# Kernel tuning notes

Hardware: AMD Instinct MI355X
Metric: run time of the kernel (lower is better)

## Reference

```python
import jax, jax.numpy as jnp
import numpy as np

STRIDE, PAD, DIL = 1, 1, 1

def _bilinear_sample(inp_flat, py, px, H, W, dtype):
    # inp_flat: [B, C, H*W]; py/px: [B, K, Ho, Wo] float sampling positions
    y0 = jnp.floor(py); x0 = jnp.floor(px)
    ly = py - y0; lx = px - x0
    y0i = y0.astype(jnp.int32); x0i = x0.astype(jnp.int32)

    def gather(yi, xi):
        valid = (yi >= 0) & (yi < H) & (xi >= 0) & (xi < W)
        idx = jnp.clip(yi, 0, H - 1) * W + jnp.clip(xi, 0, W - 1)  # [B,K,Ho,Wo]
        vals = jax.vmap(lambda xf, ix: xf[:, ix])(inp_flat, idx)    # [B,C,K,Ho,Wo]
        return vals * valid[:, None].astype(dtype)

    out = ((1 - ly) * (1 - lx))[:, None] * gather(y0i, x0i)
    out = out + ((1 - ly) * lx)[:, None] * gather(y0i, x0i + 1)
    out = out + (ly * (1 - lx))[:, None] * gather(y0i + 1, x0i)
    out = out + (ly * lx)[:, None] * gather(y0i + 1, x0i + 1)
    return out  # [B, C, K, Ho, Wo]

def setup_inputs() -> dict:
    key = jax.random.key(0)
    k1, k2, k3, k4 = jax.random.split(key, 4)
    B, Cin, Cout, H, W, kh, kw = 8, 128, 128, 64, 64, 3, 3
    n = Cin * kh * kw
    stdv = 1.0 / np.sqrt(n)
    inp = jax.random.normal(k1, (B, Cin, H, W), dtype=jnp.float32)
    offset = jax.random.normal(k2, (B, 2 * kh * kw, H, W), dtype=jnp.float32)
    mask = jax.random.uniform(k3, (B, kh * kw, H, W), dtype=jnp.float32)
    weight = jax.random.uniform(k4, (Cout, Cin, kh, kw), dtype=jnp.float32,
                                minval=-stdv, maxval=stdv)
    bias = jnp.zeros((Cout,), dtype=jnp.float32)
    return {"input": inp, "offset": offset, "mask": mask, "weight": weight, "bias": bias}

def reference(input, offset, mask, weight, bias):
    B, C, H, W = input.shape
    Cout, Cin, kh, kw = weight.shape
    K = kh * kw
    Ho = (H + 2 * PAD - DIL * (kh - 1) - 1) // STRIDE + 1
    Wo = (W + 2 * PAD - DIL * (kw - 1) - 1) // STRIDE + 1
    dtype = input.dtype

    # Offset channel layout (DCNv2): channel 2k = dy, 2k+1 = dx for kernel tap k
    off_y = offset[:, 0::2]  # [B, K, Ho, Wo]
    off_x = offset[:, 1::2]

    ky, kx = jnp.meshgrid(jnp.arange(kh), jnp.arange(kw), indexing="ij")
    ky = (ky.reshape(-1) * DIL).astype(dtype)  # [K]
    kx = (kx.reshape(-1) * DIL).astype(dtype)
    base_y = (jnp.arange(Ho) * STRIDE - PAD).astype(dtype)  # [Ho]
    base_x = (jnp.arange(Wo) * STRIDE - PAD).astype(dtype)

    py = off_y + base_y[None, None, :, None] + ky[None, :, None, None]  # [B,K,Ho,Wo]
    px = off_x + base_x[None, None, None, :] + kx[None, :, None, None]

    inp_flat = input.reshape(B, C, H * W)
    sampled = _bilinear_sample(inp_flat, py, px, H, W, dtype)  # [B,C,K,Ho,Wo]
    cols = sampled * mask[:, None]                              # modulation

    w2 = weight.reshape(Cout, Cin * K)
    cols2 = cols.reshape(B, Cin * K, Ho * Wo)
    out = jnp.einsum("om,bmp->bop", w2, cols2).reshape(B, Cout, Ho, Wo)
    return out + bias[None, :, None, None]
```

## Files before the change

### kernel.cpp

```cpp
#include <hip/hip_runtime.h>


constexpr int CIN = 128, COUT = 128, H = 64, W = 64, KK = 9;
constexpr int HW = H * W;

typedef __attribute__((ext_vector_type(8))) short short8;
typedef __attribute__((ext_vector_type(4))) float float4v;

static __device__ __forceinline__ unsigned short f32_to_bf16_rne(float f) {
  unsigned u = __float_as_uint(f);
  return (unsigned short)((u + 0x7FFFu + ((u >> 16) & 1u)) >> 16);
}
static __device__ __forceinline__ float blo(unsigned u) {
  return __uint_as_float(u << 16);
}
static __device__ __forceinline__ float bhi(unsigned u) {
  return __uint_as_float(u & 0xFFFF0000u);
}

__global__ __launch_bounds__(256) void tprep_kernel(
    const float* __restrict__ in, unsigned short* __restrict__ inT) {
  __shared__ unsigned short lt[64 * 130];
  const int b = blockIdx.x >> 6, y = blockIdx.x & 63;
  for (int i = threadIdx.x; i < 128 * 64; i += 256) {
    const int ci = i >> 6, x = i & 63;
    lt[x * 130 + ci] = f32_to_bf16_rne(in[((b * 128 + ci) * 64 + y) * 64 + x]);
  }
  __syncthreads();
  unsigned* outp = (unsigned*)inT + (size_t)(b * 64 + y) * 64 * 64;
  for (int i = threadIdx.x; i < 64 * 64; i += 256) {
    const int x = i >> 6, c2 = (i & 63) * 2;
    outp[x * 64 + (i & 63)] =
        (unsigned)lt[x * 130 + c2] | ((unsigned)lt[x * 130 + c2 + 1] << 16);
  }
}

__global__ __launch_bounds__(256) void wprep_kernel(
    const float* __restrict__ w, unsigned short* __restrict__ wt) {
  const int t = blockIdx.x * 256 + threadIdx.x;
  if (t >= 9 * 4 * 8 * 64) return;
  const int lane = t & 63, c16 = (t >> 6) & 7, kt = t >> 9;
  const int ks = kt & 3, k = kt >> 2;
  const int co = c16 * 16 + (lane & 15);
  const int ci0 = ks * 32 + (lane >> 4) * 8;
  unsigned pk[4];
#pragma unroll
  for (int jj = 0; jj < 4; ++jj) {
    const unsigned short h0 =
        f32_to_bf16_rne(w[(co * CIN + ci0 + 2 * jj) * KK + k]);
    const unsigned short h1 =
        f32_to_bf16_rne(w[(co * CIN + ci0 + 2 * jj + 1) * KK + k]);
    pk[jj] = (unsigned)h0 | ((unsigned)h1 << 16);
  }
  *(uint4*)(wt + (size_t)t * 8) = make_uint4(pk[0], pk[1], pk[2], pk[3]);
}

__global__ __launch_bounds__(256, 4) void dcn_mfma_kernel(
    const unsigned short* __restrict__ inT, const float* __restrict__ offset,
    const float* __restrict__ mask, const unsigned short* __restrict__ wt,
    const float* __restrict__ bias, float* __restrict__ out) {
  __shared__ int2 pos_i[KK * 32];
  __shared__ float4 pos_w[KK * 32];
  __shared__ unsigned short s_t[2][32 * 128];

  const int b = blockIdx.x & 7;
  const int ho = (blockIdx.x >> 3) & 63;
  const int ph = blockIdx.x >> 9;
  const int tid = threadIdx.x;

  for (int idx = tid; idx < KK * 32; idx += 256) {
    const int k = idx >> 5, p = idx & 31;
    const int pg = ph * 32 + p;
    const int ky = k / 3, kx = k - 3 * ky;
    const float py = (float)(ho - 1 + ky) +
                     offset[((b * 18 + 2 * k) * 64 + ho) * 64 + pg];
    const float px = (float)(pg - 1 + kx) +
                     offset[((b * 18 + 2 * k + 1) * 64 + ho) * 64 + pg];
    const float m = mask[((b * 9 + k) * 64 + ho) * 64 + pg];
    const float y0f = floorf(py), x0f = floorf(px);
    const int y0 = (int)y0f, x0 = (int)x0f;
    const float ly = py - y0f, lx = px - x0f;
    const float hy = 1.f - ly, hx = 1.f - lx;
    const bool vy0 = (y0 >= 0) && (y0 < H);
    const bool vy1 = (y0 + 1 >= 0) && (y0 + 1 < H);
    const bool vx0 = (x0 >= 0) && (x0 < W);
    const bool vx1 = (x0 + 1 >= 0) && (x0 + 1 < W);
    const float w00 = (vy0 && vx0) ? hy * hx * m : 0.f;
    const float w01 = (vy0 && vx1) ? hy * lx * m : 0.f;
    const float w10 = (vy1 && vx0) ? ly * hx * m : 0.f;
    const float w11 = (vy1 && vx1) ? ly * lx * m : 0.f;
    const int cy0 = min(max(y0, 0), H - 1), cy1 = min(max(y0 + 1, 0), H - 1);
    const int bx = min(max(x0, 0), W - 2);
    const int s0 = min(max(x0 - bx, 0), 1);
    const int s1 = min(max(x0 + 1 - bx, 0), 1);
    const float cA0 = (s0 == 0 ? w00 : 0.f) + (s1 == 0 ? w01 : 0.f);
    const float cB0 = (s0 == 1 ? w00 : 0.f) + (s1 == 1 ? w01 : 0.f);
    const float cA1 = (s0 == 0 ? w10 : 0.f) + (s1 == 0 ? w11 : 0.f);
    const float cB1 = (s0 == 1 ? w10 : 0.f) + (s1 == 1 ? w11 : 0.f);
    pos_i[idx] = make_int2((cy0 * 64 + bx) * 128, (cy1 * 64 + bx) * 128);
    pos_w[idx] = make_float4(cA0, cB0, cA1, cB1);
  }
  __syncthreads();

  const int wave = tid >> 6;
  const int lane = tid & 63;
  const int quad = lane >> 4, l15 = lane & 15;
  const int p_loc = tid >> 3;
  const int cg8 = tid & 7;

  float4v acc[2][2];
#pragma unroll
  for (int s = 0; s < 2; ++s)
#pragma unroll
    for (int n = 0; n < 2; ++n) acc[s][n] = (float4v)(0.f);

  const unsigned short* inb = inT + (size_t)b * HW * 128;

  int2 P = pos_i[p_loc];
  float4 Wc = pos_w[p_loc];
  uint4 ga0, ga1, gb0, gb1, gc0, gc1, gd0, gd1;
  {
    const unsigned short* a0 = inb + P.x + cg8 * 16;
    const unsigned short* a1 = inb + P.y + cg8 * 16;
    ga0 = *(const uint4*)a0;
    ga1 = *(const uint4*)(a0 + 8);
    gb0 = *(const uint4*)(a0 + 128);
    gb1 = *(const uint4*)(a0 + 136);
    gc0 = *(const uint4*)a1;
    gc1 = *(const uint4*)(a1 + 8);
    gd0 = *(const uint4*)(a1 + 128);
    gd1 = *(const uint4*)(a1 + 136);
  }

  for (int k = 0; k < KK; ++k) {
    const int buf = k & 1;
    {
      const uint4 A4[2] = {ga0, ga1}, B4[2] = {gb0, gb1};
      const uint4 C4[2] = {gc0, gc1}, D4[2] = {gd0, gd1};
#pragma unroll
      for (int h = 0; h < 2; ++h) {
        const unsigned u00[4] = {A4[h].x, A4[h].y, A4[h].z, A4[h].w};
        const unsigned u01[4] = {B4[h].x, B4[h].y, B4[h].z, B4[h].w};
        const unsigned u10[4] = {C4[h].x, C4[h].y, C4[h].z, C4[h].w};
        const unsigned u11[4] = {D4[h].x, D4[h].y, D4[h].z, D4[h].w};
        unsigned pk[4];
#pragma unroll
        for (int j = 0; j < 4; ++j) {
          const float se = Wc.x * blo(u00[j]) + Wc.y * blo(u01[j]) +
                           Wc.z * blo(u10[j]) + Wc.w * blo(u11[j]);
          const float so = Wc.x * bhi(u00[j]) + Wc.y * bhi(u01[j]) +
                           Wc.z * bhi(u10[j]) + Wc.w * bhi(u11[j]);
          pk[j] = (unsigned)f32_to_bf16_rne(se) |
                  ((unsigned)f32_to_bf16_rne(so) << 16);
        }
        const int gi = cg8 * 2 + h;
        const int pgr = gi ^ (p_loc & 7);
        *(uint4*)&s_t[buf][p_loc * 128 + pgr * 8] =
            make_uint4(pk[0], pk[1], pk[2], pk[3]);
      }
    }
    __syncthreads();

    short8 A[4][2];
    {
      const unsigned short* wk =
          wt + ((size_t)(k * 4) * 8 + wave * 2) * 512 + (size_t)lane * 8;
#pragma unroll
      for (int ks = 0; ks < 4; ++ks) {
        A[ks][0] = *(const short8*)(wk + (size_t)ks * 8 * 512);
        A[ks][1] = *(const short8*)(wk + (size_t)ks * 8 * 512 + 512);
      }
    }

    if (k < KK - 1) {
      P = pos_i[(k + 1) * 32 + p_loc];
      Wc = pos_w[(k + 1) * 32 + p_loc];
      const unsigned short* a0 = inb + P.x + cg8 * 16;
      const unsigned short* a1 = inb + P.y + cg8 * 16;
      ga0 = *(const uint4*)a0;
      ga1 = *(const uint4*)(a0 + 8);
      gb0 = *(const uint4*)(a0 + 128);
      gb1 = *(const uint4*)(a0 + 136);
      gc0 = *(const uint4*)a1;
      gc1 = *(const uint4*)(a1 + 8);
      gd0 = *(const uint4*)(a1 + 128);
      gd1 = *(const uint4*)(a1 + 136);
    }

#pragma unroll
    for (int ks = 0; ks < 4; ++ks) {
      const int gi = ks * 4 + quad;
      const int o0 = l15 * 128 + (gi ^ (l15 & 7)) * 8;
      const int o1 = (16 + l15) * 128 + (gi ^ (l15 & 7)) * 8;
      const short8 b0 = *(const short8*)&s_t[buf][o0];
      const short8 b1 = *(const short8*)&s_t[buf][o1];
      acc[0][0] =
          __builtin_amdgcn_mfma_f32_16x16x32_bf16(A[ks][0], b0, acc[0][0], 0, 0, 0);
      acc[0][1] =
          __builtin_amdgcn_mfma_f32_16x16x32_bf16(A[ks][0], b1, acc[0][1], 0, 0, 0);
      acc[1][0] =
          __builtin_amdgcn_mfma_f32_16x16x32_bf16(A[ks][1], b0, acc[1][0], 0, 0, 0);
      acc[1][1] =
          __builtin_amdgcn_mfma_f32_16x16x32_bf16(A[ks][1], b1, acc[1][1], 0, 0, 0);
    }
  }

#pragma unroll
  for (int sub = 0; sub < 2; ++sub) {
#pragma unroll
    for (int r = 0; r < 4; ++r) {
      const int co = wave * 32 + sub * 16 + quad * 4 + r;
      const float bb = bias[co];
      float* op = out + ((size_t)(b * COUT + co) * H + ho) * W + ph * 32;
      op[l15] = acc[sub][0][r] + bb;
      op[16 + l15] = acc[sub][1][r] + bb;
    }
  }
}

__global__ __launch_bounds__(256) void dcn_fp32_kernel(
    const float* __restrict__ input, const float* __restrict__ offset,
    const float* __restrict__ mask, const float* __restrict__ weight,
    const float* __restrict__ bias, float* __restrict__ out) {
  __shared__ short4 pos_o[KK * 64];
  __shared__ float4 pos_w[KK * 64];
  __shared__ float s_tile[64 * 64];
  __shared__ float w_tile[64 * 128];
  const int b = blockIdx.x >> 6;
  const int ho = blockIdx.x & 63;
  const int tid = threadIdx.x;
  for (int idx = tid; idx < KK * 64; idx += 256) {
    const int k = idx >> 6, pp = idx & 63;
    const int ky = k / 3, kx = k - 3 * ky;
    const float py = (float)(ho - 1 + ky) +
                     offset[((b * 18 + 2 * k) * 64 + ho) * 64 + pp];
    const float px = (float)(pp - 1 + kx) +
                     offset[((b * 18 + 2 * k + 1) * 64 + ho) * 64 + pp];
    const float m = mask[((b * 9 + k) * 64 + ho) * 64 + pp];
    const float y0f = floorf(py), x0f = floorf(px);
    const int y0 = (int)y0f, x0 = (int)x0f;
    const float ly = py - y0f, lx = px - x0f;
    const float hy = 1.f - ly, hx = 1.f - lx;
    const bool vy0 = (y0 >= 0) && (y0 < H), vy1 = (y0 + 1 >= 0) && (y0 + 1 < H);
    const bool vx0 = (x0 >= 0) && (x0 < W), vx1 = (x0 + 1 >= 0) && (x0 + 1 < W);
    const int cy0 = min(max(y0, 0), H - 1), cy1 = min(max(y0 + 1, 0), H - 1);
    const int cx0 = min(max(x0, 0), W - 1), cx1 = min(max(x0 + 1, 0), W - 1);
    pos_o[idx] = make_short4((short)(cy0 * W + cx0), (short)(cy0 * W + cx1),
                             (short)(cy1 * W + cx0), (short)(cy1 * W + cx1));
    pos_w[idx] = make_float4((vy0 && vx0) ? hy * hx * m : 0.f,
                             (vy0 && vx1) ? hy * lx * m : 0.f,
                             (vy1 && vx0) ? ly * hx * m : 0.f,
                             (vy1 && vx1) ? ly * lx * m : 0.f);
  }
  const int cog = tid >> 4, pg = tid & 15;
  float acc[8][4];
#pragma unroll
  for (int j = 0; j < 8; ++j)
#pragma unroll
    for (int q = 0; q < 4; ++q) acc[j][q] = 0.f;
  const float* inp_b = input + (size_t)b * CIN * HW;
  for (int k = 0; k < KK; ++k) {
    for (int cc = 0; cc < 2; ++cc) {
      __syncthreads();
      for (int i = tid; i < 64 * 64; i += 256) {
        const int cil = i >> 6, pp = i & 63;
        const float* plane = inp_b + (size_t)(cc * 64 + cil) * HW;
        const short4 o = pos_o[k * 64 + pp];
        const float4 w = pos_w[k * 64 + pp];
        s_tile[i] = w.x * plane[(int)o.x] + w.y * plane[(int)o.y] +
                    w.z * plane[(int)o.z] + w.w * plane[(int)o.w];
      }
      for (int i = tid; i < 64 * 128; i += 256) {
        const int cil = i & 63, co = i >> 6;
        w_tile[cil * 128 + co] = weight[(co * CIN + cc * 64 + cil) * KK + k];
      }
      __syncthreads();
#pragma unroll 8
      for (int cil = 0; cil < 64; ++cil) {
        const float4 sv = *(const float4*)&s_tile[cil * 64 + (pg << 2)];
        const float4 wa = *(const float4*)&w_tile[cil * 128 + (cog << 3)];
        const float4 wb = *(const float4*)&w_tile[cil * 128 + (cog << 3) + 4];
        const float s4[4] = {sv.x, sv.y, sv.z, sv.w};
        const float w8[8] = {wa.x, wa.y, wa.z, wa.w, wb.x, wb.y, wb.z, wb.w};
#pragma unroll
        for (int j = 0; j < 8; ++j)
#pragma unroll
          for (int q = 0; q < 4; ++q) acc[j][q] = fmaf(w8[j], s4[q], acc[j][q]);
      }
    }
  }
  float* outp = out + (size_t)b * COUT * HW + ho * W;
#pragma unroll
  for (int j = 0; j < 8; ++j) {
    const int co = (cog << 3) + j;
    const float bb = bias[co];
    *(float4*)&outp[co * HW + (pg << 2)] =
        make_float4(acc[j][0] + bb, acc[j][1] + bb, acc[j][2] + bb,
                    acc[j][3] + bb);
  }
}

extern "C" void kernel_launch(void* const* d_in, const int* in_sizes, int n_in,
                              void* d_out, int out_size, void* d_ws,
                              size_t ws_size, hipStream_t stream) {
  const float* input = (const float*)d_in[0];
  const float* offset = (const float*)d_in[1];
  const float* mask = (const float*)d_in[2];
  const float* weight = (const float*)d_in[3];
  const float* bias = (const float*)d_in[4];
  float* out = (float*)d_out;

  const size_t wt_bytes = (size_t)9 * 4 * 8 * 64 * 8 * 2;
  const size_t inT_bytes = (size_t)8 * HW * 128 * 2;
  if (ws_size >= wt_bytes + inT_bytes) {
    unsigned short* wt = (unsigned short*)d_ws;
    unsigned short* inT = (unsigned short*)((char*)d_ws + wt_bytes);
    hipLaunchKernelGGL(wprep_kernel, dim3(72), dim3(256), 0, stream, weight, wt);
    hipLaunchKernelGGL(tprep_kernel, dim3(512), dim3(256), 0, stream, input, inT);
    hipLaunchKernelGGL(dcn_mfma_kernel, dim3(1024), dim3(256), 0, stream, inT,
                       offset, mask, wt, bias, out);
  } else {
    hipLaunchKernelGGL(dcn_fp32_kernel, dim3(512), dim3(256), 0, stream, input,
                       offset, mask, weight, bias, out);
  }
}
```

Baseline: 107.4 us.

## Warp-specialize DCN kernel into producer sampling waves and consumer MFMA waves

Splits the block's four waves into two roles. Waves 0-1 gather and bilinearly blend the sampled input into double-buffered LDS, running one tap ahead. Waves 2-3 run the bf16 MFMA GEMM over that buffer, with each consumer wave now covering 64 output channels. The aim is to overlap gather latency with matrix math across waves rather than inside each wave. In exchange, each producer thread handles twice the gather work, each consumer thread holds twice the accumulators (more register pressure), and half the waves no longer issue MFMAs.

New measurement: 116.3 us. 1.08x slower.

```diff
diff --git a/kernel.cpp b/kernel.cpp
--- a/kernel.cpp
+++ b/kernel.cpp
@@ -103,117 +103,147 @@
   __syncthreads();
 
   const int wave = tid >> 6;
-  const int lane = tid & 63;
-  const int quad = lane >> 4, l15 = lane & 15;
-  const int p_loc = tid >> 3;
-  const int cg8 = tid & 7;
-
-  float4v acc[2][2];
-#pragma unroll
-  for (int s = 0; s < 2; ++s)
-#pragma unroll
-    for (int n = 0; n < 2; ++n) acc[s][n] = (float4v)(0.f);
-
   const unsigned short* inb = inT + (size_t)b * HW * 128;
 
-  int2 P = pos_i[p_loc];
-  float4 Wc = pos_w[p_loc];
-  uint4 ga0, ga1, gb0, gb1, gc0, gc1, gd0, gd1;
-  {
-    const unsigned short* a0 = inb + P.x + cg8 * 16;
-    const unsigned short* a1 = inb + P.y + cg8 * 16;
-    ga0 = *(const uint4*)a0;
-    ga1 = *(const uint4*)(a0 + 8);
-    gb0 = *(const uint4*)(a0 + 128);
-    gb1 = *(const uint4*)(a0 + 136);
-    gc0 = *(const uint4*)a1;
-    gc1 = *(const uint4*)(a1 + 8);
-    gd0 = *(const uint4*)(a1 + 128);
-    gd1 = *(const uint4*)(a1 + 136);
-  }
-
-  for (int k = 0; k < KK; ++k) {
-    const int buf = k & 1;
+  if (wave < 2) {
+    const int p = tid >> 2;
+    const int cgr = tid & 3;
+    const int coff = cgr * 32;
+    uint4 g00[4], g01[4], g10[4], g11[4];
+    float4 Wc;
+
     {
-      const uint4 A4[2] = {ga0, ga1}, B4[2] = {gb0, gb1};
-      const uint4 C4[2] = {gc0, gc1}, D4[2] = {gd0, gd1};
-#pragma unroll
-      for (int h = 0; h < 2; ++h) {
-        const unsigned u00[4] = {A4[h].x, A4[h].y, A4[h].z, A4[h].w};
-        const unsigned u01[4] = {B4[h].x, B4[h].y, B4[h].z, B4[h].w};
-        const unsigned u10[4] = {C4[h].x, C4[h].y, C4[h].z, C4[h].w};
-        const unsigned u11[4] = {D4[h].x, D4[h].y, D4[h].z, D4[h].w};
-        unsigned pk[4];
-#pragma unroll
-        for (int j = 0; j < 4; ++j) {
-          const float se = Wc.x * blo(u00[j]) + Wc.y * blo(u01[j]) +
-                           Wc.z * blo(u10[j]) + Wc.w * blo(u11[j]);
-          const float so = Wc.x * bhi(u00[j]) + Wc.y * bhi(u01[j]) +
-                           Wc.z * bhi(u10[j]) + Wc.w * bhi(u11[j]);
-          pk[j] = (unsigned)f32_to_bf16_rne(se) |
-                  ((unsigned)f32_to_bf16_rne(so) << 16);
+      const int2 P = pos_i[p];
+      Wc = pos_w[p];
+      const unsigned short* a0 = inb + P.x + coff;
+      const unsigned short* a1 = inb + P.y + coff;
+#pragma unroll
+      for (int q = 0; q < 4; ++q) {
+        g00[q] = *(const uint4*)(a0 + q * 8);
+        g01[q] = *(const uint4*)(a0 + 128 + q * 8);
+        g10[q] = *(const uint4*)(a1 + q * 8);
+        g11[q] = *(const uint4*)(a1 + 128 + q * 8);
+      }
+    }
+#pragma unroll
+    for (int q = 0; q < 4; ++q) {
+      const unsigned u00[4] = {g00[q].x, g00[q].y, g00[q].z, g00[q].w};
+      const unsigned u01[4] = {g01[q].x, g01[q].y, g01[q].z, g01[q].w};
+      const unsigned u10[4] = {g10[q].x, g10[q].y, g10[q].z, g10[q].w};
+      const unsigned u11[4] = {g11[q].x, g11[q].y, g11[q].z, g11[q].w};
+      unsigned pk[4];
+#pragma unroll
+      for (int c = 0; c < 4; ++c) {
+        const float se = Wc.x * blo(u00[c]) + Wc.y * blo(u01[c]) +
+                         Wc.z * blo(u10[c]) + Wc.w * blo(u11[c]);
+        const float so = Wc.x * bhi(u00[c]) + Wc.y * bhi(u01[c]) +
+                         Wc.z * bhi(u10[c]) + Wc.w * bhi(u11[c]);
+        pk[c] = (unsigned)f32_to_bf16_rne(se) |
+                ((unsigned)f32_to_bf16_rne(so) << 16);
+      }
+      const int sg = (cgr * 4 + q) ^ (p & 7);
+      *(uint4*)&s_t[0][p * 128 + sg * 8] = make_uint4(pk[0], pk[1], pk[2], pk[3]);
+    }
+    {
+      const int2 P = pos_i[32 + p];
+      Wc = pos_w[32 + p];
+      const unsigned short* a0 = inb + P.x + coff;
+      const unsigned short* a1 = inb + P.y + coff;
+#pragma unroll
+      for (int q = 0; q < 4; ++q) {
+        g00[q] = *(const uint4*)(a0 + q * 8);
+        g01[q] = *(const uint4*)(a0 + 128 + q * 8);
+        g10[q] = *(const uint4*)(a1 + q * 8);
+        g11[q] = *(const uint4*)(a1 + 128 + q * 8);
+      }
+    }
+    __syncthreads();
+
+    for (int t = 0; t < KK; ++t) {
+      if (t < KK - 1) {
+#pragma unroll
+        for (int q = 0; q < 4; ++q) {
+          const unsigned u00[4] = {g00[q].x, g00[q].y, g00[q].z, g00[q].w};
+          const unsigned u01[4] = {g01[q].x, g01[q].y, g01[q].z, g01[q].w};
+          const unsigned u10[4] = {g10[q].x, g10[q].y, g10[q].z, g10[q].w};
+          const unsigned u11[4] = {g11[q].x, g11[q].y, g11[q].z, g11[q].w};
+          unsigned pk[4];
+#pragma unroll
+          for (int c = 0; c < 4; ++c) {
+            const float se = Wc.x * blo(u00[c]) + Wc.y * blo(u01[c]) +
+                             Wc.z * blo(u10[c]) + Wc.w * blo(u11[c]);
+            const float so = Wc.x * bhi(u00[c]) + Wc.y * bhi(u01[c]) +
+                             Wc.z * bhi(u10[c]) + Wc.w * bhi(u11[c]);
+            pk[c] = (unsigned)f32_to_bf16_rne(se) |
+                    ((unsigned)f32_to_bf16_rne(so) << 16);
+          }
+          const int sg = (cgr * 4 + q) ^ (p & 7);
+          *(uint4*)&s_t[(t + 1) & 1][p * 128 + sg * 8] =
+              make_uint4(pk[0], pk[1], pk[2], pk[3]);
         }
-        const int gi = cg8 * 2 + h;
-        const int pgr = gi ^ (p_loc & 7);
-        *(uint4*)&s_t[buf][p_loc * 128 + pgr * 8] =
-            make_uint4(pk[0], pk[1], pk[2], pk[3]);
-      }
-    }
+        if (t < KK - 2) {
+          const int2 P = pos_i[(t + 2) * 32 + p];
+          Wc = pos_w[(t + 2) * 32 + p];
+          const unsigned short* a0 = inb + P.x + coff;
+          const unsigned short* a1 = inb + P.y + coff;
+#pragma unroll
+          for (int q = 0; q < 4; ++q) {
+            g00[q] = *(const uint4*)(a0 + q * 8);
+            g01[q] = *(const uint4*)(a0 + 128 + q * 8);
+            g10[q] = *(const uint4*)(a1 + q * 8);
+            g11[q] = *(const uint4*)(a1 + 128 + q * 8);
+          }
+        }
+      }
+      __syncthreads();
+    }
+  } else {
+    const int cw = wave - 2;
+    const int lane = tid & 63;
+    const int quad = lane >> 4, l15 = lane & 15;
+
+    float4v acc[4][2];
+#pragma unroll
+    for (int s = 0; s < 4; ++s)
+#pragma unroll
+      for (int n = 0; n < 2; ++n) acc[s][n] = (float4v)(0.f);
+
     __syncthreads();
 
-    short8 A[4][2];
-    {
-      const unsigned short* wk =
-          wt + ((size_t)(k * 4) * 8 + wave * 2) * 512 + (size_t)lane * 8;
+    for (int t = 0; t < KK; ++t) {
+      const int buf = t & 1;
+      const unsigned short* wkbase =
+          wt + ((size_t)t * 32 + cw * 4) * 512 + (size_t)lane * 8;
 #pragma unroll
       for (int ks = 0; ks < 4; ++ks) {
-        A[ks][0] = *(const short8*)(wk + (size_t)ks * 8 * 512);
-        A[ks][1] = *(const short8*)(wk + (size_t)ks * 8 * 512 + 512);
-      }
-    }
-
-    if (k < KK - 1) {
-      P = pos_i[(k + 1) * 32 + p_loc];
-      Wc = pos_w[(k + 1) * 32 + p_loc];
-      const unsigned short* a0 = inb + P.x + cg8 * 16;
-      const unsigned short* a1 = inb + P.y + cg8 * 16;
-      ga0 = *(const uint4*)a0;
-      ga1 = *(const uint4*)(a0 + 8);
-      gb0 = *(const uint4*)(a0 + 128);
-      gb1 = *(const uint4*)(a0 + 136);
-      gc0 = *(const uint4*)a1;
-      gc1 = *(const uint4*)(a1 + 8);
-      gd0 = *(const uint4*)(a1 + 128);
-      gd1 = *(const uint4*)(a1 + 136);
-    }
-
-#pragma unroll
-    for (int ks = 0; ks < 4; ++ks) {
-      const int gi = ks * 4 + quad;
-      const int o0 = l15 * 128 + (gi ^ (l15 & 7)) * 8;
-      const int o1 = (16 + l15) * 128 + (gi ^ (l15 & 7)) * 8;
-      const short8 b0 = *(const short8*)&s_t[buf][o0];
-      const short8 b1 = *(const short8*)&s_t[buf][o1];
-      acc[0][0] =
-          __builtin_amdgcn_mfma_f32_16x16x32_bf16(A[ks][0], b0, acc[0][0], 0, 0, 0);
-      acc[0][1] =
-          __builtin_amdgcn_mfma_f32_16x16x32_bf16(A[ks][0], b1, acc[0][1], 0, 0, 0);
-      acc[1][0] =
-          __builtin_amdgcn_mfma_f32_16x16x32_bf16(A[ks][1], b0, acc[1][0], 0, 0, 0);
-      acc[1][1] =
-          __builtin_amdgcn_mfma_f32_16x16x32_bf16(A[ks][1], b1, acc[1][1], 0, 0, 0);
-    }
-  }
-
-#pragma unroll
-  for (int sub = 0; sub < 2; ++sub) {
-#pragma unroll
-    for (int r = 0; r < 4; ++r) {
-      const int co = wave * 32 + sub * 16 + quad * 4 + r;
-      const float bb = bias[co];
-      float* op = out + ((size_t)(b * COUT + co) * H + ho) * W + ph * 32;
-      op[l15] = acc[sub][0][r] + bb;
-      op[16 + l15] = acc[sub][1][r] + bb;
+        short8 A[4];
+#pragma unroll
+        for (int sub = 0; sub < 4; ++sub)
+          A[sub] = *(const short8*)(wkbase + (size_t)(ks * 8 + sub) * 512);
+        const int swz = ((ks * 4 + quad) ^ (l15 & 7)) * 8;
+        const short8 b0 = *(const short8*)&s_t[buf][l15 * 128 + swz];
+        const short8 b1 = *(const short8*)&s_t[buf][(16 + l15) * 128 + swz];
+#pragma unroll
+        for (int sub = 0; sub < 4; ++sub) {
+          acc[sub][0] = __builtin_amdgcn_mfma_f32_16x16x32_bf16(A[sub], b0,
+                                                               acc[sub][0], 0, 0, 0);
+          acc[sub][1] = __builtin_amdgcn_mfma_f32_16x16x32_bf16(A[sub], b1,
+                                                               acc[sub][1], 0, 0, 0);
+        }
+      }
+      __syncthreads();
+    }
+
+#pragma unroll
+    for (int sub = 0; sub < 4; ++sub) {
+#pragma unroll
+      for (int r = 0; r < 4; ++r) {
+        const int co = cw * 64 + sub * 16 + quad * 4 + r;
+        const float bb = bias[co];
+        float* op = out + ((size_t)(b * COUT + co) * H + ho) * W + ph * 32;
+        op[l15] = acc[sub][0][r] + bb;
+        op[16 + l15] = acc[sub][1][r] + bb;
+      }
     }
   }
 }
```

## Widen DCN MFMA block to full output row with 8 waves

Applied to the files above, without the earlier changes.

Each block now handles a full 64-pixel output row using 512 threads (8 waves) instead of half a row with 256 threads. Each wave computes 16 output channels across all 64 pixels, so it loads half as many weight fragments per tap while covering twice the pixels. The sampling and position tables are shared across the whole row, which halves redundant per-block setup and the block count. The trade-off is more shared memory per block, a smaller grid and fewer independent accumulators per wave, which may lower occupancy or latency hiding.

Measured after the change: 104.9 us. 2.4% less time.

```diff
diff --git a/kernel.cpp b/kernel.cpp
--- a/kernel.cpp
+++ b/kernel.cpp
@@ -55,28 +55,26 @@
   *(uint4*)(wt + (size_t)t * 8) = make_uint4(pk[0], pk[1], pk[2], pk[3]);
 }
 
-__global__ __launch_bounds__(256, 4) void dcn_mfma_kernel(
+__global__ __launch_bounds__(512, 4) void dcn_mfma_kernel(
     const unsigned short* __restrict__ inT, const float* __restrict__ offset,
     const float* __restrict__ mask, const unsigned short* __restrict__ wt,
     const float* __restrict__ bias, float* __restrict__ out) {
-  __shared__ int2 pos_i[KK * 32];
-  __shared__ float4 pos_w[KK * 32];
-  __shared__ unsigned short s_t[2][32 * 128];
+  __shared__ int2 pos_i[KK * 64];
+  __shared__ float4 pos_w[KK * 64];
+  __shared__ unsigned short s_t[2][64 * 128];
 
   const int b = blockIdx.x & 7;
-  const int ho = (blockIdx.x >> 3) & 63;
-  const int ph = blockIdx.x >> 9;
+  const int ho = blockIdx.x >> 3;
   const int tid = threadIdx.x;
 
-  for (int idx = tid; idx < KK * 32; idx += 256) {
-    const int k = idx >> 5, p = idx & 31;
-    const int pg = ph * 32 + p;
+  for (int idx = tid; idx < KK * 64; idx += 512) {
+    const int k = idx >> 6, p = idx & 63;
     const int ky = k / 3, kx = k - 3 * ky;
     const float py = (float)(ho - 1 + ky) +
-                     offset[((b * 18 + 2 * k) * 64 + ho) * 64 + pg];
-    const float px = (float)(pg - 1 + kx) +
-                     offset[((b * 18 + 2 * k + 1) * 64 + ho) * 64 + pg];
-    const float m = mask[((b * 9 + k) * 64 + ho) * 64 + pg];
+                     offset[((b * 18 + 2 * k) * 64 + ho) * 64 + p];
+    const float px = (float)(p - 1 + kx) +
+                     offset[((b * 18 + 2 * k + 1) * 64 + ho) * 64 + p];
+    const float m = mask[((b * 9 + k) * 64 + ho) * 64 + p];
     const float y0f = floorf(py), x0f = floorf(px);
     const int y0 = (int)y0f, x0 = (int)x0f;
     const float ly = py - y0f, lx = px - x0f;
@@ -108,11 +106,9 @@
   const int p_loc = tid >> 3;
   const int cg8 = tid & 7;
 
-  float4v acc[2][2];
-#pragma unroll
-  for (int s = 0; s < 2; ++s)
-#pragma unroll
-    for (int n = 0; n < 2; ++n) acc[s][n] = (float4v)(0.f);
+  float4v acc[4];
+#pragma unroll
+  for (int n = 0; n < 4; ++n) acc[n] = (float4v)(0.f);
 
   const unsigned short* inb = inT + (size_t)b * HW * 128;
 
@@ -161,20 +157,19 @@
     }
     __syncthreads();
 
-    short8 A[4][2];
+    short8 A0, A1, A2, A3;
     {
       const unsigned short* wk =
-          wt + ((size_t)(k * 4) * 8 + wave * 2) * 512 + (size_t)lane * 8;
-#pragma unroll
-      for (int ks = 0; ks < 4; ++ks) {
-        A[ks][0] = *(const short8*)(wk + (size_t)ks * 8 * 512);
-        A[ks][1] = *(const short8*)(wk + (size_t)ks * 8 * 512 + 512);
-      }
+          wt + ((size_t)(k * 4) * 8 + wave) * 512 + (size_t)lane * 8;
+      A0 = *(const short8*)(wk);
+      A1 = *(const short8*)(wk + 8 * 512);
+      A2 = *(const short8*)(wk + 16 * 512);
+      A3 = *(const short8*)(wk + 24 * 512);
     }
 
     if (k < KK - 1) {
-      P = pos_i[(k + 1) * 32 + p_loc];
-      Wc = pos_w[(k + 1) * 32 + p_loc];
+      P = pos_i[(k + 1) * 64 + p_loc];
+      Wc = pos_w[(k + 1) * 64 + p_loc];
       const unsigned short* a0 = inb + P.x + cg8 * 16;
       const unsigned short* a1 = inb + P.y + cg8 * 16;
       ga0 = *(const uint4*)a0;
@@ -189,32 +184,25 @@
 
 #pragma unroll
     for (int ks = 0; ks < 4; ++ks) {
+      const short8 Ak = (ks == 0) ? A0 : (ks == 1) ? A1 : (ks == 2) ? A2 : A3;
       const int gi = ks * 4 + quad;
-      const int o0 = l15 * 128 + (gi ^ (l15 & 7)) * 8;
-      const int o1 = (16 + l15) * 128 + (gi ^ (l15 & 7)) * 8;
-      const short8 b0 = *(const short8*)&s_t[buf][o0];
-      const short8 b1 = *(const short8*)&s_t[buf][o1];
-      acc[0][0] =
-          __builtin_amdgcn_mfma_f32_16x16x32_bf16(A[ks][0], b0, acc[0][0], 0, 0, 0);
-      acc[0][1] =
-          __builtin_amdgcn_mfma_f32_16x16x32_bf16(A[ks][0], b1, acc[0][1], 0, 0, 0);
-      acc[1][0] =
-          __builtin_amdgcn_mfma_f32_16x16x32_bf16(A[ks][1], b0, acc[1][0], 0, 0, 0);
-      acc[1][1] =
-          __builtin_amdgcn_mfma_f32_16x16x32_bf16(A[ks][1], b1, acc[1][1], 0, 0, 0);
-    }
-  }
-
-#pragma unroll
-  for (int sub = 0; sub < 2; ++sub) {
-#pragma unroll
-    for (int r = 0; r < 4; ++r) {
-      const int co = wave * 32 + sub * 16 + quad * 4 + r;
-      const float bb = bias[co];
-      float* op = out + ((size_t)(b * COUT + co) * H + ho) * W + ph * 32;
-      op[l15] = acc[sub][0][r] + bb;
-      op[16 + l15] = acc[sub][1][r] + bb;
-    }
+#pragma unroll
+      for (int ns = 0; ns < 4; ++ns) {
+        const int row = ns * 16 + l15;
+        const short8 Bn =
+            *(const short8*)&s_t[buf][row * 128 + (gi ^ (row & 7)) * 8];
+        acc[ns] = __builtin_amdgcn_mfma_f32_16x16x32_bf16(Ak, Bn, acc[ns], 0, 0, 0);
+      }
+    }
+  }
+
+#pragma unroll
+  for (int r = 0; r < 4; ++r) {
+    const int co = wave * 16 + quad * 4 + r;
+    const float bb = bias[co];
+    float* op = out + ((size_t)(b * COUT + co) * H + ho) * W;
+#pragma unroll
+    for (int ns = 0; ns < 4; ++ns) op[ns * 16 + l15] = acc[ns][r] + bb;
   }
 }
 
@@ -317,7 +305,7 @@
     unsigned short* inT = (unsigned short*)((char*)d_ws + wt_bytes);
     hipLaunchKernelGGL(wprep_kernel, dim3(72), dim3(256), 0, stream, weight, wt);
     hipLaunchKernelGGL(tprep_kernel, dim3(512), dim3(256), 0, stream, input, inT);
-    hipLaunchKernelGGL(dcn_mfma_kernel, dim3(1024), dim3(256), 0, stream, inT,
+    hipLaunchKernelGGL(dcn_mfma_kernel, dim3(512), dim3(512), 0, stream, inT,
                        offset, mask, wt, bias, out);
   } else {
     hipLaunchKernelGGL(dcn_fp32_kernel, dim3(512), dim3(256), 0, stream, input,
```
